# Performance work log

Measured on AMD Instinct MI355X. Metric: run time of the kernel, lower is better.

Reference implementation:

```python
import jax, jax.numpy as jnp
import numpy as np

B, T, V, E, H, NC = 256, 512, 128, 128, 256, 10000


def setup_inputs() -> dict:
    key = jax.random.key(0)
    ks = jax.random.split(key, 10)
    return {
        "dec_input_batch": jax.random.randint(ks[0], (B, T), 0, V),
        "dec_input_lengths": jax.random.randint(ks[1], (B,), 1, T + 1),
        "max_prob_clusters": jax.random.randint(ks[2], (B,), 0, NC),
        "char_embeddings": jax.random.normal(ks[3], (V, E), dtype=jnp.float32) * 0.1,
        "cluster_embeddings": jax.random.normal(ks[4], (NC, H), dtype=jnp.float32) * 0.1,
        "W0": jax.random.normal(ks[5], (E + H + H, 4 * H), dtype=jnp.float32) * 0.05,
        "b0": jnp.zeros((4 * H,), jnp.float32),
        "W1": jax.random.normal(ks[6], (H + H, 4 * H), dtype=jnp.float32) * 0.05,
        "b1": jnp.zeros((4 * H,), jnp.float32),
        "decoderW": jax.random.normal(ks[7], (H, V), dtype=jnp.float32) * (1.0 / (H + V)),
        "decoderB": jnp.zeros((V,), jnp.float32),
    }


def _lstm_step(c, h, x, W, b):
    # TF BasicLSTMCell: gates order i, j, f, o; forget_bias = 1.0
    z = jnp.concatenate([x, h], axis=-1) @ W + b
    i, j, f, o = jnp.split(z, 4, axis=-1)
    c2 = c * jax.nn.sigmoid(f + 1.0) + jax.nn.sigmoid(i) * jnp.tanh(j)
    h2 = jnp.tanh(c2) * jax.nn.sigmoid(o)
    return c2, h2


def reference(dec_input_batch, dec_input_lengths, max_prob_clusters,
              char_embeddings, cluster_embeddings, W0, b0, W1, b1,
              decoderW, decoderB):
    Bb, Tt = dec_input_batch.shape
    Hh = decoderW.shape[0]
    x = char_embeddings[dec_input_batch]                       # [B,T,E]
    clus = cluster_embeddings[max_prob_clusters]               # [B,H]
    clus_bt = jnp.broadcast_to(clus[:, None, :], (Bb, Tt, clus.shape[-1]))
    x = jnp.concatenate([x, clus_bt], axis=-1)                 # [B,T,E+H]
    xs = jnp.transpose(x, (1, 0, 2))                           # [T,B,E+H]
    # dynamic_rnn sequence_length semantics: past length -> zero output, state copied through
    mask = (jnp.arange(Tt)[:, None] < dec_input_lengths[None, :])[..., None]  # [T,B,1]
    zeros = jnp.zeros((Bb, Hh), x.dtype)

    def step(carry, inp):
        c0, h0, c1, h1 = carry
        xt, m = inp
        c0n, h0n = _lstm_step(c0, h0, xt, W0, b0)
        c1n, h1n = _lstm_step(c1, h1, h0n, W1, b1)
        c0 = jnp.where(m, c0n, c0); h0 = jnp.where(m, h0n, h0)
        c1 = jnp.where(m, c1n, c1); h1 = jnp.where(m, h1n, h1)
        out = jnp.where(m, h1n, jnp.zeros_like(h1n))
        return (c0, h0, c1, h1), out

    _, outs = jax.lax.scan(step, (zeros, zeros, zeros, zeros), (xs, mask))
    outs = jnp.transpose(outs, (1, 0, 2))                      # [B,T,H]
    raw_scores = outs @ decoderW + decoderB                    # [B,T,V]
    return raw_scores
```

## Files before the change

### kernel.cpp

```cpp
#include <hip/hip_runtime.h>

#define B_ 256
#define T_ 512
#define V_ 128
#define E_ 128
#define H_ 256
#define FH 1024

#define GROUPS 32
#define RPG 8
#define CWG 16
#define NWG (GROUPS*CWG)

#define HTG (H_*RPG)
#define GST (GROUPS*HTG)

typedef float f4 __attribute__((ext_vector_type(4)));

#define OFF_HT0  0
#define OFF_HT1  (OFF_HT0 + 2*GST)
#define OFF_BAR  (OFF_HT1 + 2*GST)
#define OFF_TP   (OFF_BAR + 4096)
#define OFF_CP   (OFF_TP + V_*FH)
#define OFF_WP0  (OFF_CP + B_*FH)
#define OFF_WP1  (OFF_WP0 + CWG*64*64*4)
#define OFF_DWT  (OFF_WP1 + CWG*128*64*4)
#define OFF_B1   (OFF_DWT + V_*H_)

__device__ __forceinline__ int gcol(int c, int col) {
  int u = col >> 2, g = col & 3;
  return g*256 + c*16 + u;
}

__device__ __forceinline__ float sigm(float x){ return 1.f/(1.f+__expf(-x)); }
__device__ __forceinline__ float tanh_(float x){ return 1.f - 2.f/(1.f+__expf(2.f*x)); }


__global__ void prep_pack(const float* __restrict__ W0, const float* __restrict__ W1,
                          const float* __restrict__ dW, const float* __restrict__ b1,
                          float* __restrict__ ws) {
  float* wp0 = ws + OFF_WP0; float* wp1 = ws + OFF_WP1;
  float* dwT = ws + OFF_DWT; float* b1p = ws + OFF_B1;
  const int N0 = CWG*64*64*4;
  const int N1 = CWG*128*64*4;
  const int N2 = V_*H_;
  const int N3 = FH;
  const int total = N0+N1+N2+N3;
  for (int i = blockIdx.x*blockDim.x + threadIdx.x; i < total; i += gridDim.x*blockDim.x) {
    if (i < N0) {
      int cc = i >> 14; int rem = i & 16383;
      int kb = rem >> 8; int ln = (rem >> 2) & 63; int j = i & 3;
      int k = kb*4 + j;
      wp0[i] = W0[(E_+H_+k)*FH + gcol(cc, ln)];
    } else if (i < N0+N1) {
      int idx = i - N0;
      int cc = idx >> 15; int rem = idx & 32767;
      int kb = rem >> 8; int ln = (rem >> 2) & 63; int j = idx & 3;
      int k2 = kb*4 + j;
      wp1[idx] = W1[k2*FH + gcol(cc, ln)];
    } else if (i < N0+N1+N2) {
      int l = i - N0 - N1;
      int v = l >> 8, k = l & 255;
      dwT[l] = dW[k*V_ + v];
    } else {
      int cc2 = i - N0 - N1 - N2;
      b1p[cc2] = b1[gcol(cc2>>6, cc2&63)];
    }
  }
}

__global__ void prep_tok(const float* __restrict__ cemb, const float* __restrict__ W0,
                         float* __restrict__ ws) {
  __shared__ float ce[E_];
  float* TP = ws + OFF_TP;
  int v = blockIdx.x >> 2, q = blockIdx.x & 3;
  int tid = threadIdx.x;
  if (tid < E_) ce[tid] = cemb[v*E_ + tid];
  __syncthreads();
  int ccol = q*256 + tid;
  int G = gcol(ccol>>6, ccol&63);
  float acc = 0.f;
  for (int e = 0; e < E_; ++e) acc = fmaf(ce[e], W0[e*FH + G], acc);
  TP[v*FH + ccol] = acc;
}

__global__ void prep_clus(const int* __restrict__ clus, const float* __restrict__ clemb,
                          const float* __restrict__ W0, const float* __restrict__ b0,
                          float* __restrict__ ws) {
  __shared__ float ce[H_];
  float* CP = ws + OFF_CP;
  int b = blockIdx.x >> 2, q = blockIdx.x & 3;
  int tid = threadIdx.x;
  int cl = clus[b];
  ce[tid] = clemb[(long long)cl*H_ + tid];
  __syncthreads();
  int ccol = q*256 + tid;
  int G = gcol(ccol>>6, ccol&63);
  float acc = b0[G];
  for (int e = 0; e < H_; ++e) acc = fmaf(ce[e], W0[(E_+e)*FH + G], acc);
  CP[b*FH + ccol] = acc;
}


__device__ __forceinline__ void st_coh(float* p, float v) {
  __hip_atomic_store(p, v, __ATOMIC_RELAXED, __HIP_MEMORY_SCOPE_AGENT);
}

__device__ __forceinline__ void stage_row(const float* g, float* l) {
  const unsigned long long* p = (const unsigned long long*)g;
  unsigned long long d0 = __hip_atomic_load(p+0, __ATOMIC_RELAXED, __HIP_MEMORY_SCOPE_AGENT);
  unsigned long long d1 = __hip_atomic_load(p+1, __ATOMIC_RELAXED, __HIP_MEMORY_SCOPE_AGENT);
  unsigned long long d2 = __hip_atomic_load(p+2, __ATOMIC_RELAXED, __HIP_MEMORY_SCOPE_AGENT);
  unsigned long long d3 = __hip_atomic_load(p+3, __ATOMIC_RELAXED, __HIP_MEMORY_SCOPE_AGENT);
  float2 f0 = __builtin_bit_cast(float2, d0);
  float2 f1 = __builtin_bit_cast(float2, d1);
  float2 f2 = __builtin_bit_cast(float2, d2);
  float2 f3 = __builtin_bit_cast(float2, d3);
  f4 lo = {f0.x, f0.y, f1.x, f1.y};
  f4 hi = {f2.x, f2.y, f3.x, f3.y};
  *(f4*)(l)     = lo;
  *(f4*)(l + 4) = hi;
}

__device__ __forceinline__ void flag_set(unsigned* p, unsigned v) {
  asm volatile("s_waitcnt vmcnt(0)" ::: "memory");
  __hip_atomic_store(p, v, __ATOMIC_RELAXED, __HIP_MEMORY_SCOPE_AGENT);
}

__device__ __forceinline__ void spinAB(const unsigned* fA, const unsigned* fB,
                                       int lane, unsigned tgt) {
  const unsigned* p = ((lane < 32) ? fA : fB) + (lane & 15);
  unsigned v = __hip_atomic_load(p, __ATOMIC_RELAXED, __HIP_MEMORY_SCOPE_AGENT);
  while (!__all((int)(v >= tgt))) {
    __builtin_amdgcn_s_sleep(2);
    v = __hip_atomic_load(p, __ATOMIC_RELAXED, __HIP_MEMORY_SCOPE_AGENT);
  }
}

__device__ __forceinline__ void spin1(const unsigned* f, int lane, unsigned tgt) {
  const unsigned* p = f + (lane & 15);
  unsigned v = __hip_atomic_load(p, __ATOMIC_RELAXED, __HIP_MEMORY_SCOPE_AGENT);
  while (!__all((int)(v >= tgt))) {
    __builtin_amdgcn_s_sleep(2);
    v = __hip_atomic_load(p, __ATOMIC_RELAXED, __HIP_MEMORY_SCOPE_AGENT);
  }
}

__device__ __forceinline__ void lstm_gate(const f4 z, float& cc, float& hh, const bool upd) {
  float ci = sigm(z.x);
  float cj = tanh_(z.y);
  float cf = sigm(z.z + 1.f);
  float co = sigm(z.w);
  float cn = fmaf(cc, cf, ci*cj);
  float hn = tanh_(cn)*co;
  if (upd) { cc = cn; hh = hn; }
}


__global__ __launch_bounds__(256, 2) void lstm_persist(
    const int* __restrict__ toks, const int* __restrict__ lens,
    const float* __restrict__ decB, float* __restrict__ ws, float* __restrict__ out)
{
  const int blk  = blockIdx.x;
  const int grp  = ((blk & 7) << 2) | ((blk >> 3) >> 4);
  const int c    = (blk >> 3) & 15;
  const int tid  = threadIdx.x;
  const int lane = tid & 63;
  const int wv   = tid >> 6;
  const int cof  = c*64;

  float* ht0 = ws + OFF_HT0;
  float* ht1 = ws + OFF_HT1;
  unsigned* fgrp = (unsigned*)(ws + OFF_BAR) + grp*128;
  unsigned* fA = fgrp;
  unsigned* fB = fgrp + 32;
  const float* TP   = ws + OFF_TP;
  const float* CP   = ws + OFF_CP;
  const float* wp0c = ws + OFF_WP0 + c*(64*64*4);
  const float* wp1c = ws + OFF_WP1 + c*(128*64*4);
  const float* dwT  = ws + OFF_DWT;
  const float* b1p  = ws + OFF_B1;

  __shared__ __align__(16) float h0s[256][8];
  __shared__ __align__(16) float h1s[256][8];
  __shared__ float za[4][8][64];
  __shared__ float zb[4][8][64];
  __shared__ float ldsW[8][260];
  __shared__ float pred[4][64];

  for (int i = tid; i < 8*H_; i += 256)
    ldsW[i>>8][i&255] = dwT[(c*8 + (i>>8))*H_ + (i&255)];

  const int sk = (tid + (c << 4)) & 255;

  int Lg = lens[grp*RPG + (lane & 7)];
  Lg = max(Lg, __shfl_xor(Lg, 1));
  Lg = max(Lg, __shfl_xor(Lg, 2));
  Lg = max(Lg, __shfl_xor(Lg, 4));

  const int gu = lane & 15, q = lane >> 4;
  const int rowA = grp*RPG + q, rowB = grp*RPG + q + 4;
  const int lenA = lens[rowA], lenB = lens[rowB];
  const int* tokApt = toks + rowA*T_;
  const int* tokBpt = toks + rowB*T_;
  const f4 cpA = *(const f4*)(CP + rowA*FH + cof + gu*4);
  const f4 cpB = *(const f4*)(CP + rowB*FH + cof + gu*4);
  const f4 b1v = *(const f4*)(b1p + cof + gu*4);
  const int puboff = grp*HTG + (c*16 + gu)*8;
  float c0A = 0.f, h0A = 0.f, c0B = 0.f, h0B = 0.f;
  float c1A = 0.f, h1A = 0.f, c1B = 0.f, h1B = 0.f;

  const int pm = lane >> 3, pv = lane & 7;
  const int plen = lens[grp*RPG + pm];
  const float decb = decB[c*8 + pv];
  float* outp = out + (size_t)(grp*RPG + pm)*T_*V_ + c*8 + pv;

  float a0[8], a1[8];

  __syncthreads();

  if (wv == 0) {
    int tokA = tokApt[0], tokB = tokBpt[0];
    f4 zA = *(const f4*)(TP + tokA*FH + cof + gu*4) + cpA;
    f4 zB = *(const f4*)(TP + tokB*FH + cof + gu*4) + cpB;
    lstm_gate(zA, c0A, h0A, 0 < lenA);
    lstm_gate(zB, c0B, h0B, 0 < lenB);
    float* pb = ht0 + puboff;
    st_coh(pb + q,     h0A);
    st_coh(pb + q + 4, h0B);
    if (lane == 0) flag_set(fA + c, 1u);
  } else if (wv == 1) {
    if (lane == 0) flag_set(fB + c, 1u);
  }

  for (int t = 0; t < Lg; ++t) {
    const int buf = t & 1;

    if (wv == 0) spinAB(fA, fB, lane, (unsigned)(t + 1));
    __syncthreads();
    __atomic_signal_fence(__ATOMIC_SEQ_CST);

    f4 tpA = {0.f,0.f,0.f,0.f}, tpB = {0.f,0.f,0.f,0.f};
    if (wv == 0 && t + 1 < Lg) {
      tpA = *(const f4*)(TP + tokApt[t+1]*FH + cof + gu*4);
      tpB = *(const f4*)(TP + tokBpt[t+1]*FH + cof + gu*4);
    }

    stage_row(ht0 + buf*GST + grp*HTG + sk*8, &h0s[sk][0]);
    stage_row(ht1 + buf*GST + grp*HTG + sk*8, &h1s[sk][0]);
    __syncthreads();

    #pragma unroll
    for (int r = 0; r < 8; ++r) { a0[r] = 0.f; a1[r] = 0.f; }
    #pragma unroll 2
    for (int b = 0; b < 16; ++b) {
      const int kb = wv*16 + b;
      const f4 w0  = *(const f4*)(wp0c + kb*256 + lane*4);
      const f4 wlo = *(const f4*)(wp1c + kb*256 + lane*4);
      const f4 wup = *(const f4*)(wp1c + (64 + kb)*256 + lane*4);
      const float* w0a  = (const float*)&w0;
      const float* wloa = (const float*)&wlo;
      const float* wupa = (const float*)&wup;
      #pragma unroll
      for (int j = 0; j < 4; ++j) {
        const int k = kb*4 + j;
        const f4 h0a = *(const f4*)&h0s[k][0];
        const f4 h0b = *(const f4*)&h0s[k][4];
        const f4 h1a = *(const f4*)&h1s[k][0];
        const f4 h1b = *(const f4*)&h1s[k][4];
        const float w0j = w0a[j], wlj = wloa[j], wuj = wupa[j];
        a0[0]=fmaf(w0j,h0a.x,a0[0]); a0[1]=fmaf(w0j,h0a.y,a0[1]);
        a0[2]=fmaf(w0j,h0a.z,a0[2]); a0[3]=fmaf(w0j,h0a.w,a0[3]);
        a0[4]=fmaf(w0j,h0b.x,a0[4]); a0[5]=fmaf(w0j,h0b.y,a0[5]);
        a0[6]=fmaf(w0j,h0b.z,a0[6]); a0[7]=fmaf(w0j,h0b.w,a0[7]);
        a1[0]=fmaf(wlj,h0a.x,a1[0]); a1[1]=fmaf(wlj,h0a.y,a1[1]);
        a1[2]=fmaf(wlj,h0a.z,a1[2]); a1[3]=fmaf(wlj,h0a.w,a1[3]);
        a1[4]=fmaf(wlj,h0b.x,a1[4]); a1[5]=fmaf(wlj,h0b.y,a1[5]);
        a1[6]=fmaf(wlj,h0b.z,a1[6]); a1[7]=fmaf(wlj,h0b.w,a1[7]);
        a1[0]=fmaf(wuj,h1a.x,a1[0]); a1[1]=fmaf(wuj,h1a.y,a1[1]);
        a1[2]=fmaf(wuj,h1a.z,a1[2]); a1[3]=fmaf(wuj,h1a.w,a1[3]);
        a1[4]=fmaf(wuj,h1b.x,a1[4]); a1[5]=fmaf(wuj,h1b.y,a1[5]);
        a1[6]=fmaf(wuj,h1b.z,a1[6]); a1[7]=fmaf(wuj,h1b.w,a1[7]);
      }
    }

    float pacc = 0.f;
    {
      const int kq = wv*64;
      #pragma unroll 4
      for (int k2 = 0; k2 < 64; k2 += 4) {
        const f4 w4 = *(const f4*)&ldsW[pv][kq + k2];
        pacc = fmaf(h1s[kq+k2  ][pm], w4.x, pacc);
        pacc = fmaf(h1s[kq+k2+1][pm], w4.y, pacc);
        pacc = fmaf(h1s[kq+k2+2][pm], w4.z, pacc);
        pacc = fmaf(h1s[kq+k2+3][pm], w4.w, pacc);
      }
    }

    #pragma unroll
    for (int r = 0; r < 8; ++r) { za[wv][r][lane] = a0[r]; zb[wv][r][lane] = a1[r]; }
    pred[wv][lane] = pacc;
    __syncthreads();

    if (wv == 0) {
      if (t + 1 < Lg) {
        f4 sA = *(const f4*)&za[0][q][gu*4];
        sA += *(const f4*)&za[1][q][gu*4];
        sA += *(const f4*)&za[2][q][gu*4];
        sA += *(const f4*)&za[3][q][gu*4];
        f4 sB = *(const f4*)&za[0][q+4][gu*4];
        sB += *(const f4*)&za[1][q+4][gu*4];
        sB += *(const f4*)&za[2][q+4][gu*4];
        sB += *(const f4*)&za[3][q+4][gu*4];
        f4 zA = sA + tpA + cpA;
        f4 zB = sB + tpB + cpB;
        lstm_gate(zA, c0A, h0A, (t+1) < lenA);
        lstm_gate(zB, c0B, h0B, (t+1) < lenB);
        float* pb = ht0 + (buf^1)*GST + puboff;
        st_coh(pb + q,     h0A);
        st_coh(pb + q + 4, h0B);
        if (lane == 0) flag_set(fA + c, (unsigned)(t + 2));
      }
    } else if (wv == 1) {
      f4 sA = *(const f4*)&zb[0][q][gu*4];
      sA += *(const f4*)&zb[1][q][gu*4];
      sA += *(const f4*)&zb[2][q][gu*4];
      sA += *(const f4*)&zb[3][q][gu*4];
      f4 sB = *(const f4*)&zb[0][q+4][gu*4];
      sB += *(const f4*)&zb[1][q+4][gu*4];
      sB += *(const f4*)&zb[2][q+4][gu*4];
      sB += *(const f4*)&zb[3][q+4][gu*4];
      f4 zA = sA + b1v;
      f4 zB = sB + b1v;
      lstm_gate(zA, c1A, h1A, t < lenA);
      lstm_gate(zB, c1B, h1B, t < lenB);
      float* pb = ht1 + (buf^1)*GST + puboff;
      st_coh(pb + q,     h1A);
      st_coh(pb + q + 4, h1B);
      if (lane == 0) flag_set(fB + c, (unsigned)(t + 2));
    } else if (wv == 2) {
      if (t > 0) {
        float tot = pred[0][lane] + pred[1][lane] + pred[2][lane] + pred[3][lane] + decb;
        if (t - 1 < plen) outp[(size_t)(t-1)*V_] = tot;
      }
    }
  }

  if (wv == 0) spin1(fB, lane, (unsigned)(Lg + 1));
  __syncthreads();
  __atomic_signal_fence(__ATOMIC_SEQ_CST);
  stage_row(ht1 + (Lg & 1)*GST + grp*HTG + sk*8, &h1s[sk][0]);
  __syncthreads();
  {
    float pacc = 0.f;
    const int kq = wv*64;
    #pragma unroll 4
    for (int k2 = 0; k2 < 64; k2 += 4) {
      const f4 w4 = *(const f4*)&ldsW[pv][kq + k2];
      pacc = fmaf(h1s[kq+k2  ][pm], w4.x, pacc);
      pacc = fmaf(h1s[kq+k2+1][pm], w4.y, pacc);
      pacc = fmaf(h1s[kq+k2+2][pm], w4.z, pacc);
      pacc = fmaf(h1s[kq+k2+3][pm], w4.w, pacc);
    }
    pred[wv][lane] = pacc;
  }
  __syncthreads();
  if (wv == 2) {
    float tot = pred[0][lane] + pred[1][lane] + pred[2][lane] + pred[3][lane] + decb;
    if (Lg - 1 < plen) outp[(size_t)(Lg-1)*V_] = tot;
  }
}


extern "C" void kernel_launch(void* const* d_in, const int* in_sizes, int n_in,
                              void* d_out, int out_size, void* d_ws, size_t ws_size,
                              hipStream_t stream) {
  const int*   toks  = (const int*)d_in[0];
  const int*   lens  = (const int*)d_in[1];
  const int*   clus  = (const int*)d_in[2];
  const float* cemb  = (const float*)d_in[3];
  const float* clemb = (const float*)d_in[4];
  const float* W0    = (const float*)d_in[5];
  const float* b0    = (const float*)d_in[6];
  const float* W1    = (const float*)d_in[7];
  const float* b1    = (const float*)d_in[8];
  const float* dW    = (const float*)d_in[9];
  const float* decB  = (const float*)d_in[10];
  float* out = (float*)d_out;
  float* ws  = (float*)d_ws;

  hipMemsetAsync(out, 0, (size_t)B_*T_*V_*sizeof(float), stream);
  hipMemsetAsync(ws, 0, (size_t)(OFF_BAR + 4096)*sizeof(float), stream);

  prep_pack<<<1024, 256, 0, stream>>>(W0, W1, dW, b1, ws);
  prep_tok <<<V_*4, 256, 0, stream>>>(cemb, W0, ws);
  prep_clus<<<B_*4, 256, 0, stream>>>(clus, clemb, W0, b0, ws);
  lstm_persist<<<NWG, 256, 0, stream>>>(toks, lens, decB, ws, out);
}
```

Before: 5.507 ms.

## Split batch into 64 groups of 4 rows across 1024 persistent workgroups

Halves the rows each workgroup handles, from 8 to 4, and doubles the number of groups and workgroups from 512 to 1024. Occupancy rises to 4 blocks per CU, and the LDS staging, accumulators and output projection shrink to match. The aim is to shorten the serial per-timestep critical path by giving each block half the FMA work. Because each group now takes the max sequence length over only 4 rows, short groups also stop their recurrence earlier. In exchange, every block streams the per-column weight slice each step, so twice as many blocks read weights. The persistent spin-wait scheme also now depends on all 1024 blocks being co-resident.

Result: slower. 6.797 ms (+23.4%).

```diff
diff --git a/kernel.cpp b/kernel.cpp
--- a/kernel.cpp
+++ b/kernel.cpp
@@ -7,8 +7,8 @@
 #define H_ 256
 #define FH 1024
 
-#define GROUPS 32
-#define RPG 8
+#define GROUPS 64
+#define RPG 4
 #define CWG 16
 #define NWG (GROUPS*CWG)
 
@@ -20,7 +20,8 @@
 #define OFF_HT0  0
 #define OFF_HT1  (OFF_HT0 + 2*GST)
 #define OFF_BAR  (OFF_HT1 + 2*GST)
-#define OFF_TP   (OFF_BAR + 4096)
+#define BARSZ    (GROUPS*128)
+#define OFF_TP   (OFF_BAR + BARSZ)
 #define OFF_CP   (OFF_TP + V_*FH)
 #define OFF_WP0  (OFF_CP + B_*FH)
 #define OFF_WP1  (OFF_WP0 + CWG*64*64*4)
@@ -106,20 +107,14 @@
   __hip_atomic_store(p, v, __ATOMIC_RELAXED, __HIP_MEMORY_SCOPE_AGENT);
 }
 
-__device__ __forceinline__ void stage_row(const float* g, float* l) {
+__device__ __forceinline__ void stage16(const float* g, float* l) {
   const unsigned long long* p = (const unsigned long long*)g;
   unsigned long long d0 = __hip_atomic_load(p+0, __ATOMIC_RELAXED, __HIP_MEMORY_SCOPE_AGENT);
   unsigned long long d1 = __hip_atomic_load(p+1, __ATOMIC_RELAXED, __HIP_MEMORY_SCOPE_AGENT);
-  unsigned long long d2 = __hip_atomic_load(p+2, __ATOMIC_RELAXED, __HIP_MEMORY_SCOPE_AGENT);
-  unsigned long long d3 = __hip_atomic_load(p+3, __ATOMIC_RELAXED, __HIP_MEMORY_SCOPE_AGENT);
   float2 f0 = __builtin_bit_cast(float2, d0);
   float2 f1 = __builtin_bit_cast(float2, d1);
-  float2 f2 = __builtin_bit_cast(float2, d2);
-  float2 f3 = __builtin_bit_cast(float2, d3);
-  f4 lo = {f0.x, f0.y, f1.x, f1.y};
-  f4 hi = {f2.x, f2.y, f3.x, f3.y};
-  *(f4*)(l)     = lo;
-  *(f4*)(l + 4) = hi;
+  f4 v = {f0.x, f0.y, f1.x, f1.y};
+  *(f4*)(l) = v;
 }
 
 __device__ __forceinline__ void flag_set(unsigned* p, unsigned v) {
@@ -157,13 +152,13 @@
 }
 
 
-__global__ __launch_bounds__(256, 2) void lstm_persist(
+__global__ __launch_bounds__(256, 4) void lstm_persist(
     const int* __restrict__ toks, const int* __restrict__ lens,
     const float* __restrict__ decB, float* __restrict__ ws, float* __restrict__ out)
 {
   const int blk  = blockIdx.x;
-  const int grp  = ((blk & 7) << 2) | ((blk >> 3) >> 4);
-  const int c    = (blk >> 3) & 15;
+  const int grp  = (blk & 7)*8 + ((blk >> 3) & 7);
+  const int c    = blk >> 6;
   const int tid  = threadIdx.x;
   const int lane = tid & 63;
   const int wv   = tid >> 6;
@@ -181,53 +176,46 @@
   const float* dwT  = ws + OFF_DWT;
   const float* b1p  = ws + OFF_B1;
 
-  __shared__ __align__(16) float h0s[256][8];
-  __shared__ __align__(16) float h1s[256][8];
-  __shared__ float za[4][8][64];
-  __shared__ float zb[4][8][64];
+  __shared__ __align__(16) float h0s[256][4];
+  __shared__ __align__(16) float h1s[256][4];
+  __shared__ float za[4][4][64];
+  __shared__ float zb[4][4][64];
   __shared__ float ldsW[8][260];
-  __shared__ float pred[4][64];
+  __shared__ float pred[8][32];
 
   for (int i = tid; i < 8*H_; i += 256)
     ldsW[i>>8][i&255] = dwT[(c*8 + (i>>8))*H_ + (i&255)];
 
   const int sk = (tid + (c << 4)) & 255;
 
-  int Lg = lens[grp*RPG + (lane & 7)];
+  int Lg = lens[grp*RPG + (lane & 3)];
   Lg = max(Lg, __shfl_xor(Lg, 1));
   Lg = max(Lg, __shfl_xor(Lg, 2));
-  Lg = max(Lg, __shfl_xor(Lg, 4));
 
   const int gu = lane & 15, q = lane >> 4;
-  const int rowA = grp*RPG + q, rowB = grp*RPG + q + 4;
-  const int lenA = lens[rowA], lenB = lens[rowB];
+  const int rowA = grp*RPG + q;
+  const int lenA = lens[rowA];
   const int* tokApt = toks + rowA*T_;
-  const int* tokBpt = toks + rowB*T_;
   const f4 cpA = *(const f4*)(CP + rowA*FH + cof + gu*4);
-  const f4 cpB = *(const f4*)(CP + rowB*FH + cof + gu*4);
   const f4 b1v = *(const f4*)(b1p + cof + gu*4);
-  const int puboff = grp*HTG + (c*16 + gu)*8;
-  float c0A = 0.f, h0A = 0.f, c0B = 0.f, h0B = 0.f;
-  float c1A = 0.f, h1A = 0.f, c1B = 0.f, h1B = 0.f;
-
-  const int pm = lane >> 3, pv = lane & 7;
+  const int puboff = grp*HTG + (c*16 + gu)*4 + q;
+  float c0A = 0.f, h0A = 0.f;
+  float c1A = 0.f, h1A = 0.f;
+
+  const int half = lane >> 5, pm = (lane >> 3) & 3, pv = lane & 7;
   const int plen = lens[grp*RPG + pm];
   const float decb = decB[c*8 + pv];
   float* outp = out + (size_t)(grp*RPG + pm)*T_*V_ + c*8 + pv;
 
-  float a0[8], a1[8];
+  float a0[4], a1[4];
 
   __syncthreads();
 
   if (wv == 0) {
-    int tokA = tokApt[0], tokB = tokBpt[0];
+    int tokA = tokApt[0];
     f4 zA = *(const f4*)(TP + tokA*FH + cof + gu*4) + cpA;
-    f4 zB = *(const f4*)(TP + tokB*FH + cof + gu*4) + cpB;
     lstm_gate(zA, c0A, h0A, 0 < lenA);
-    lstm_gate(zB, c0B, h0B, 0 < lenB);
-    float* pb = ht0 + puboff;
-    st_coh(pb + q,     h0A);
-    st_coh(pb + q + 4, h0B);
+    st_coh(ht0 + puboff, h0A);
     if (lane == 0) flag_set(fA + c, 1u);
   } else if (wv == 1) {
     if (lane == 0) flag_set(fB + c, 1u);
@@ -240,18 +228,16 @@
     __syncthreads();
     __atomic_signal_fence(__ATOMIC_SEQ_CST);
 
-    f4 tpA = {0.f,0.f,0.f,0.f}, tpB = {0.f,0.f,0.f,0.f};
-    if (wv == 0 && t + 1 < Lg) {
+    f4 tpA = {0.f,0.f,0.f,0.f};
+    if (wv == 0 && t + 1 < Lg)
       tpA = *(const f4*)(TP + tokApt[t+1]*FH + cof + gu*4);
-      tpB = *(const f4*)(TP + tokBpt[t+1]*FH + cof + gu*4);
-    }
-
-    stage_row(ht0 + buf*GST + grp*HTG + sk*8, &h0s[sk][0]);
-    stage_row(ht1 + buf*GST + grp*HTG + sk*8, &h1s[sk][0]);
+
+    stage16(ht0 + buf*GST + grp*HTG + sk*4, &h0s[sk][0]);
+    stage16(ht1 + buf*GST + grp*HTG + sk*4, &h1s[sk][0]);
     __syncthreads();
 
     #pragma unroll
-    for (int r = 0; r < 8; ++r) { a0[r] = 0.f; a1[r] = 0.f; }
+    for (int r = 0; r < 4; ++r) { a0[r] = 0.f; a1[r] = 0.f; }
     #pragma unroll 2
     for (int b = 0; b < 16; ++b) {
       const int kb = wv*16 + b;
@@ -264,31 +250,23 @@
       #pragma unroll
       for (int j = 0; j < 4; ++j) {
         const int k = kb*4 + j;
-        const f4 h0a = *(const f4*)&h0s[k][0];
-        const f4 h0b = *(const f4*)&h0s[k][4];
-        const f4 h1a = *(const f4*)&h1s[k][0];
-        const f4 h1b = *(const f4*)&h1s[k][4];
+        const f4 h0v = *(const f4*)&h0s[k][0];
+        const f4 h1v = *(const f4*)&h1s[k][0];
         const float w0j = w0a[j], wlj = wloa[j], wuj = wupa[j];
-        a0[0]=fmaf(w0j,h0a.x,a0[0]); a0[1]=fmaf(w0j,h0a.y,a0[1]);
-        a0[2]=fmaf(w0j,h0a.z,a0[2]); a0[3]=fmaf(w0j,h0a.w,a0[3]);
-        a0[4]=fmaf(w0j,h0b.x,a0[4]); a0[5]=fmaf(w0j,h0b.y,a0[5]);
-        a0[6]=fmaf(w0j,h0b.z,a0[6]); a0[7]=fmaf(w0j,h0b.w,a0[7]);
-        a1[0]=fmaf(wlj,h0a.x,a1[0]); a1[1]=fmaf(wlj,h0a.y,a1[1]);
-        a1[2]=fmaf(wlj,h0a.z,a1[2]); a1[3]=fmaf(wlj,h0a.w,a1[3]);
-        a1[4]=fmaf(wlj,h0b.x,a1[4]); a1[5]=fmaf(wlj,h0b.y,a1[5]);
-        a1[6]=fmaf(wlj,h0b.z,a1[6]); a1[7]=fmaf(wlj,h0b.w,a1[7]);
-        a1[0]=fmaf(wuj,h1a.x,a1[0]); a1[1]=fmaf(wuj,h1a.y,a1[1]);
-        a1[2]=fmaf(wuj,h1a.z,a1[2]); a1[3]=fmaf(wuj,h1a.w,a1[3]);
-        a1[4]=fmaf(wuj,h1b.x,a1[4]); a1[5]=fmaf(wuj,h1b.y,a1[5]);
-        a1[6]=fmaf(wuj,h1b.z,a1[6]); a1[7]=fmaf(wuj,h1b.w,a1[7]);
+        a0[0]=fmaf(w0j,h0v.x,a0[0]); a0[1]=fmaf(w0j,h0v.y,a0[1]);
+        a0[2]=fmaf(w0j,h0v.z,a0[2]); a0[3]=fmaf(w0j,h0v.w,a0[3]);
+        a1[0]=fmaf(wlj,h0v.x,a1[0]); a1[1]=fmaf(wlj,h0v.y,a1[1]);
+        a1[2]=fmaf(wlj,h0v.z,a1[2]); a1[3]=fmaf(wlj,h0v.w,a1[3]);
+        a1[0]=fmaf(wuj,h1v.x,a1[0]); a1[1]=fmaf(wuj,h1v.y,a1[1]);
+        a1[2]=fmaf(wuj,h1v.z,a1[2]); a1[3]=fmaf(wuj,h1v.w,a1[3]);
       }
     }
 
     float pacc = 0.f;
     {
-      const int kq = wv*64;
-      #pragma unroll 4
-      for (int k2 = 0; k2 < 64; k2 += 4) {
+      const int kq = wv*64 + half*32;
+      #pragma unroll 8
+      for (int k2 = 0; k2 < 32; k2 += 4) {
         const f4 w4 = *(const f4*)&ldsW[pv][kq + k2];
         pacc = fmaf(h1s[kq+k2  ][pm], w4.x, pacc);
         pacc = fmaf(h1s[kq+k2+1][pm], w4.y, pacc);
@@ -298,8 +276,8 @@
     }
 
     #pragma unroll
-    for (int r = 0; r < 8; ++r) { za[wv][r][lane] = a0[r]; zb[wv][r][lane] = a1[r]; }
-    pred[wv][lane] = pacc;
+    for (int r = 0; r < 4; ++r) { za[wv][r][lane] = a0[r]; zb[wv][r][lane] = a1[r]; }
+    pred[wv*2 + half][lane & 31] = pacc;
     __syncthreads();
 
     if (wv == 0) {
@@ -308,17 +286,9 @@
         sA += *(const f4*)&za[1][q][gu*4];
         sA += *(const f4*)&za[2][q][gu*4];
         sA += *(const f4*)&za[3][q][gu*4];
-        f4 sB = *(const f4*)&za[0][q+4][gu*4];
-        sB += *(const f4*)&za[1][q+4][gu*4];
-        sB += *(const f4*)&za[2][q+4][gu*4];
-        sB += *(const f4*)&za[3][q+4][gu*4];
         f4 zA = sA + tpA + cpA;
-        f4 zB = sB + tpB + cpB;
         lstm_gate(zA, c0A, h0A, (t+1) < lenA);
-        lstm_gate(zB, c0B, h0B, (t+1) < lenB);
-        float* pb = ht0 + (buf^1)*GST + puboff;
-        st_coh(pb + q,     h0A);
-        st_coh(pb + q + 4, h0B);
+        st_coh(ht0 + (buf^1)*GST + puboff, h0A);
         if (lane == 0) flag_set(fA + c, (unsigned)(t + 2));
       }
     } else if (wv == 1) {
@@ -326,21 +296,15 @@
       sA += *(const f4*)&zb[1][q][gu*4];
       sA += *(const f4*)&zb[2][q][gu*4];
       sA += *(const f4*)&zb[3][q][gu*4];
-      f4 sB = *(const f4*)&zb[0][q+4][gu*4];
-      sB += *(const f4*)&zb[1][q+4][gu*4];
-      sB += *(const f4*)&zb[2][q+4][gu*4];
-      sB += *(const f4*)&zb[3][q+4][gu*4];
       f4 zA = sA + b1v;
-      f4 zB = sB + b1v;
       lstm_gate(zA, c1A, h1A, t < lenA);
-      lstm_gate(zB, c1B, h1B, t < lenB);
-      float* pb = ht1 + (buf^1)*GST + puboff;
-      st_coh(pb + q,     h1A);
-      st_coh(pb + q + 4, h1B);
+      st_coh(ht1 + (buf^1)*GST + puboff, h1A);
       if (lane == 0) flag_set(fB + c, (unsigned)(t + 2));
     } else if (wv == 2) {
-      if (t > 0) {
-        float tot = pred[0][lane] + pred[1][lane] + pred[2][lane] + pred[3][lane] + decb;
+      if (t > 0 && lane < 32) {
+        float tot = decb;
+        #pragma unroll
+        for (int p = 0; p < 8; ++p) tot += pred[p][lane];
         if (t - 1 < plen) outp[(size_t)(t-1)*V_] = tot;
       }
     }
@@ -349,24 +313,26 @@
   if (wv == 0) spin1(fB, lane, (unsigned)(Lg + 1));
   __syncthreads();
   __atomic_signal_fence(__ATOMIC_SEQ_CST);
-  stage_row(ht1 + (Lg & 1)*GST + grp*HTG + sk*8, &h1s[sk][0]);
+  stage16(ht1 + (Lg & 1)*GST + grp*HTG + sk*4, &h1s[sk][0]);
   __syncthreads();
   {
     float pacc = 0.f;
-    const int kq = wv*64;
-    #pragma unroll 4
-    for (int k2 = 0; k2 < 64; k2 += 4) {
+    const int kq = wv*64 + half*32;
+    #pragma unroll 8
+    for (int k2 = 0; k2 < 32; k2 += 4) {
       const f4 w4 = *(const f4*)&ldsW[pv][kq + k2];
       pacc = fmaf(h1s[kq+k2  ][pm], w4.x, pacc);
       pacc = fmaf(h1s[kq+k2+1][pm], w4.y, pacc);
       pacc = fmaf(h1s[kq+k2+2][pm], w4.z, pacc);
       pacc = fmaf(h1s[kq+k2+3][pm], w4.w, pacc);
     }
-    pred[wv][lane] = pacc;
-  }
-  __syncthreads();
-  if (wv == 2) {
-    float tot = pred[0][lane] + pred[1][lane] + pred[2][lane] + pred[3][lane] + decb;
+    pred[wv*2 + half][lane & 31] = pacc;
+  }
+  __syncthreads();
+  if (wv == 2 && lane < 32) {
+    float tot = decb;
+    #pragma unroll
+    for (int p = 0; p < 8; ++p) tot += pred[p][lane];
     if (Lg - 1 < plen) outp[(size_t)(Lg-1)*V_] = tot;
   }
 }
@@ -390,7 +356,7 @@
   float* ws  = (float*)d_ws;
 
   hipMemsetAsync(out, 0, (size_t)B_*T_*V_*sizeof(float), stream);
-  hipMemsetAsync(ws, 0, (size_t)(OFF_BAR + 4096)*sizeof(float), stream);
+  hipMemsetAsync(ws, 0, (size_t)(OFF_BAR + BARSZ)*sizeof(float), stream);
 
   prep_pack<<<1024, 256, 0, stream>>>(W0, W1, dW, b1, ws);
   prep_tok <<<V_*4, 256, 0, stream>>>(cemb, W0, ws);
```

## Pad flags to separate lines, drop staging barrier, pack h publishes into 64-bit stores

Applied to the files above, without the earlier changes.

Each per-column readiness flag for layer 0 and layer 1 now sits on its own cache line instead of sharing one. Hidden-state publishes pack the two batch rows into a single 64-bit atomic store. Each wave stages from global memory exactly the slice of h it later reads, which removes the __syncthreads between staging and the matvec. The next-token table loads are issued before the spin-wait, and the spin sleep is lengthened. The aim is less false sharing and polling traffic, fewer barriers and fewer stores on the serial per-step critical path, at the cost of a larger flag region and coarser polling granularity.

Measured after the change: 5.421 ms. About the same (-1.6%).

```diff
diff --git a/kernel.cpp b/kernel.cpp
--- a/kernel.cpp
+++ b/kernel.cpp
@@ -12,7 +12,7 @@
 #define CWG 16
 #define NWG (GROUPS*CWG)
 
-#define HTG (H_*RPG)
+#define HTG 2048
 #define GST (GROUPS*HTG)
 
 typedef float f4 __attribute__((ext_vector_type(4)));
@@ -20,7 +20,8 @@
 #define OFF_HT0  0
 #define OFF_HT1  (OFF_HT0 + 2*GST)
 #define OFF_BAR  (OFF_HT1 + 2*GST)
-#define OFF_TP   (OFF_BAR + 4096)
+#define BARSZ    (GROUPS*1024)
+#define OFF_TP   (OFF_BAR + BARSZ)
 #define OFF_CP   (OFF_TP + V_*FH)
 #define OFF_WP0  (OFF_CP + B_*FH)
 #define OFF_WP1  (OFF_WP0 + CWG*64*64*4)
@@ -102,24 +103,15 @@
 }
 
 
-__device__ __forceinline__ void st_coh(float* p, float v) {
-  __hip_atomic_store(p, v, __ATOMIC_RELAXED, __HIP_MEMORY_SCOPE_AGENT);
-}
-
-__device__ __forceinline__ void stage_row(const float* g, float* l) {
-  const unsigned long long* p = (const unsigned long long*)g;
-  unsigned long long d0 = __hip_atomic_load(p+0, __ATOMIC_RELAXED, __HIP_MEMORY_SCOPE_AGENT);
-  unsigned long long d1 = __hip_atomic_load(p+1, __ATOMIC_RELAXED, __HIP_MEMORY_SCOPE_AGENT);
-  unsigned long long d2 = __hip_atomic_load(p+2, __ATOMIC_RELAXED, __HIP_MEMORY_SCOPE_AGENT);
-  unsigned long long d3 = __hip_atomic_load(p+3, __ATOMIC_RELAXED, __HIP_MEMORY_SCOPE_AGENT);
-  float2 f0 = __builtin_bit_cast(float2, d0);
-  float2 f1 = __builtin_bit_cast(float2, d1);
-  float2 f2 = __builtin_bit_cast(float2, d2);
-  float2 f3 = __builtin_bit_cast(float2, d3);
-  f4 lo = {f0.x, f0.y, f1.x, f1.y};
-  f4 hi = {f2.x, f2.y, f3.x, f3.y};
-  *(f4*)(l)     = lo;
-  *(f4*)(l + 4) = hi;
+__device__ __forceinline__ void st64(float* p, float a, float b) {
+  float2 t; t.x = a; t.y = b;
+  __hip_atomic_store((unsigned long long*)p, __builtin_bit_cast(unsigned long long, t),
+                     __ATOMIC_RELAXED, __HIP_MEMORY_SCOPE_AGENT);
+}
+
+__device__ __forceinline__ unsigned long long ld64(const void* p) {
+  return __hip_atomic_load((const unsigned long long*)p, __ATOMIC_RELAXED,
+                           __HIP_MEMORY_SCOPE_AGENT);
 }
 
 __device__ __forceinline__ void flag_set(unsigned* p, unsigned v) {
@@ -127,21 +119,20 @@
   __hip_atomic_store(p, v, __ATOMIC_RELAXED, __HIP_MEMORY_SCOPE_AGENT);
 }
 
-__device__ __forceinline__ void spinAB(const unsigned* fA, const unsigned* fB,
-                                       int lane, unsigned tgt) {
-  const unsigned* p = ((lane < 32) ? fA : fB) + (lane & 15);
+__device__ __forceinline__ void spinAB(const unsigned* fgrp, int lane, unsigned tgt) {
+  const unsigned* p = fgrp + (lane & 15)*32 + ((lane >> 5) << 4);
   unsigned v = __hip_atomic_load(p, __ATOMIC_RELAXED, __HIP_MEMORY_SCOPE_AGENT);
   while (!__all((int)(v >= tgt))) {
-    __builtin_amdgcn_s_sleep(2);
+    __builtin_amdgcn_s_sleep(4);
     v = __hip_atomic_load(p, __ATOMIC_RELAXED, __HIP_MEMORY_SCOPE_AGENT);
   }
 }
 
-__device__ __forceinline__ void spin1(const unsigned* f, int lane, unsigned tgt) {
-  const unsigned* p = f + (lane & 15);
+__device__ __forceinline__ void spinB(const unsigned* fgrp, int lane, unsigned tgt) {
+  const unsigned* p = fgrp + (lane & 15)*32 + 16;
   unsigned v = __hip_atomic_load(p, __ATOMIC_RELAXED, __HIP_MEMORY_SCOPE_AGENT);
   while (!__all((int)(v >= tgt))) {
-    __builtin_amdgcn_s_sleep(2);
+    __builtin_amdgcn_s_sleep(4);
     v = __hip_atomic_load(p, __ATOMIC_RELAXED, __HIP_MEMORY_SCOPE_AGENT);
   }
 }
@@ -162,7 +153,7 @@
     const float* __restrict__ decB, float* __restrict__ ws, float* __restrict__ out)
 {
   const int blk  = blockIdx.x;
-  const int grp  = ((blk & 7) << 2) | ((blk >> 3) >> 4);
+  const int grp  = ((blk & 7) << 2) | (blk >> 7);
   const int c    = (blk >> 3) & 15;
   const int tid  = threadIdx.x;
   const int lane = tid & 63;
@@ -171,9 +162,7 @@
 
   float* ht0 = ws + OFF_HT0;
   float* ht1 = ws + OFF_HT1;
-  unsigned* fgrp = (unsigned*)(ws + OFF_BAR) + grp*128;
-  unsigned* fA = fgrp;
-  unsigned* fB = fgrp + 32;
+  unsigned* fgrp = (unsigned*)(ws + OFF_BAR) + grp*1024;
   const float* TP   = ws + OFF_TP;
   const float* CP   = ws + OFF_CP;
   const float* wp0c = ws + OFF_WP0 + c*(64*64*4);
@@ -181,17 +170,15 @@
   const float* dwT  = ws + OFF_DWT;
   const float* b1p  = ws + OFF_B1;
 
-  __shared__ __align__(16) float h0s[256][8];
-  __shared__ __align__(16) float h1s[256][8];
-  __shared__ float za[4][8][64];
-  __shared__ float zb[4][8][64];
+  __shared__ __align__(16) float h0s[2048];
+  __shared__ __align__(16) float h1s[2048];
+  __shared__ __align__(16) float za[4][8][64];
+  __shared__ __align__(16) float zb[4][8][64];
   __shared__ float ldsW[8][260];
   __shared__ float pred[4][64];
 
   for (int i = tid; i < 8*H_; i += 256)
     ldsW[i>>8][i&255] = dwT[(c*8 + (i>>8))*H_ + (i&255)];
-
-  const int sk = (tid + (c << 4)) & 255;
 
   int Lg = lens[grp*RPG + (lane & 7)];
   Lg = max(Lg, __shfl_xor(Lg, 1));
@@ -206,81 +193,77 @@
   const f4 cpA = *(const f4*)(CP + rowA*FH + cof + gu*4);
   const f4 cpB = *(const f4*)(CP + rowB*FH + cof + gu*4);
   const f4 b1v = *(const f4*)(b1p + cof + gu*4);
-  const int puboff = grp*HTG + (c*16 + gu)*8;
+  const int puboff = grp*HTG + (c*16 + gu)*8 + q*2;
   float c0A = 0.f, h0A = 0.f, c0B = 0.f, h0B = 0.f;
   float c1A = 0.f, h1A = 0.f, c1B = 0.f, h1B = 0.f;
 
   const int pm = lane >> 3, pv = lane & 7;
+  const int prm = (pm < 4) ? pm*2 : (pm-4)*2 + 1;
   const int plen = lens[grp*RPG + pm];
   const float decb = decB[c*8 + pv];
   float* outp = out + (size_t)(grp*RPG + pm)*T_*V_ + c*8 + pv;
 
-  float a0[8], a1[8];
-
   __syncthreads();
 
   if (wv == 0) {
-    int tokA = tokApt[0], tokB = tokBpt[0];
-    f4 zA = *(const f4*)(TP + tokA*FH + cof + gu*4) + cpA;
-    f4 zB = *(const f4*)(TP + tokB*FH + cof + gu*4) + cpB;
-    lstm_gate(zA, c0A, h0A, 0 < lenA);
-    lstm_gate(zB, c0B, h0B, 0 < lenB);
-    float* pb = ht0 + puboff;
-    st_coh(pb + q,     h0A);
-    st_coh(pb + q + 4, h0B);
-    if (lane == 0) flag_set(fA + c, 1u);
+    f4 zAv = *(const f4*)(TP + tokApt[0]*FH + cof + gu*4) + cpA;
+    f4 zBv = *(const f4*)(TP + tokBpt[0]*FH + cof + gu*4) + cpB;
+    lstm_gate(zAv, c0A, h0A, 0 < lenA);
+    lstm_gate(zBv, c0B, h0B, 0 < lenB);
+    st64(ht0 + puboff, h0A, h0B);
+    if (lane == 0) flag_set(fgrp + c*32, 1u);
   } else if (wv == 1) {
-    if (lane == 0) flag_set(fB + c, 1u);
+    if (lane == 0) flag_set(fgrp + c*32 + 16, 1u);
   }
 
   for (int t = 0; t < Lg; ++t) {
     const int buf = t & 1;
 
-    if (wv == 0) spinAB(fA, fB, lane, (unsigned)(t + 1));
-    __syncthreads();
-    __atomic_signal_fence(__ATOMIC_SEQ_CST);
-
-    f4 tpA = {0.f,0.f,0.f,0.f}, tpB = {0.f,0.f,0.f,0.f};
+    f4 tpA = {0,0,0,0}, tpB = {0,0,0,0};
     if (wv == 0 && t + 1 < Lg) {
       tpA = *(const f4*)(TP + tokApt[t+1]*FH + cof + gu*4);
       tpB = *(const f4*)(TP + tokBpt[t+1]*FH + cof + gu*4);
     }
 
-    stage_row(ht0 + buf*GST + grp*HTG + sk*8, &h0s[sk][0]);
-    stage_row(ht1 + buf*GST + grp*HTG + sk*8, &h1s[sk][0]);
+    if (wv == 0) spinAB(fgrp, lane, (unsigned)(t + 1));
     __syncthreads();
-
-    #pragma unroll
-    for (int r = 0; r < 8; ++r) { a0[r] = 0.f; a1[r] = 0.f; }
+    __atomic_signal_fence(__ATOMIC_SEQ_CST);
+
+    {
+      const float* s0 = ht0 + buf*GST + grp*HTG + wv*512 + lane*8;
+      const float* s1 = ht1 + buf*GST + grp*HTG + wv*512 + lane*8;
+      unsigned long long a0 = ld64(s0),   a1 = ld64(s0+2);
+      unsigned long long a2 = ld64(s0+4), a3 = ld64(s0+6);
+      unsigned long long b0 = ld64(s1),   b1 = ld64(s1+2);
+      unsigned long long b2 = ld64(s1+4), b3 = ld64(s1+6);
+      float* d0 = h0s + wv*512 + lane*8;
+      float* d1 = h1s + wv*512 + lane*8;
+      *(unsigned long long*)(d0)   = a0; *(unsigned long long*)(d0+2) = a1;
+      *(unsigned long long*)(d0+4) = a2; *(unsigned long long*)(d0+6) = a3;
+      *(unsigned long long*)(d1)   = b0; *(unsigned long long*)(d1+2) = b1;
+      *(unsigned long long*)(d1+4) = b2; *(unsigned long long*)(d1+6) = b3;
+    }
+
+    f4 A0l = {0,0,0,0}, A0h = {0,0,0,0}, A1l = {0,0,0,0}, A1h = {0,0,0,0};
     #pragma unroll 2
     for (int b = 0; b < 16; ++b) {
       const int kb = wv*16 + b;
-      const f4 w0  = *(const f4*)(wp0c + kb*256 + lane*4);
-      const f4 wlo = *(const f4*)(wp1c + kb*256 + lane*4);
-      const f4 wup = *(const f4*)(wp1c + (64 + kb)*256 + lane*4);
-      const float* w0a  = (const float*)&w0;
-      const float* wloa = (const float*)&wlo;
-      const float* wupa = (const float*)&wup;
+      const f4 w0 = *(const f4*)(wp0c + kb*256 + lane*4);
+      const f4 wl = *(const f4*)(wp1c + kb*256 + lane*4);
+      const f4 wu = *(const f4*)(wp1c + (64 + kb)*256 + lane*4);
       #pragma unroll
       for (int j = 0; j < 4; ++j) {
         const int k = kb*4 + j;
-        const f4 h0a = *(const f4*)&h0s[k][0];
-        const f4 h0b = *(const f4*)&h0s[k][4];
-        const f4 h1a = *(const f4*)&h1s[k][0];
-        const f4 h1b = *(const f4*)&h1s[k][4];
-        const float w0j = w0a[j], wlj = wloa[j], wuj = wupa[j];
-        a0[0]=fmaf(w0j,h0a.x,a0[0]); a0[1]=fmaf(w0j,h0a.y,a0[1]);
-        a0[2]=fmaf(w0j,h0a.z,a0[2]); a0[3]=fmaf(w0j,h0a.w,a0[3]);
-        a0[4]=fmaf(w0j,h0b.x,a0[4]); a0[5]=fmaf(w0j,h0b.y,a0[5]);
-        a0[6]=fmaf(w0j,h0b.z,a0[6]); a0[7]=fmaf(w0j,h0b.w,a0[7]);
-        a1[0]=fmaf(wlj,h0a.x,a1[0]); a1[1]=fmaf(wlj,h0a.y,a1[1]);
-        a1[2]=fmaf(wlj,h0a.z,a1[2]); a1[3]=fmaf(wlj,h0a.w,a1[3]);
-        a1[4]=fmaf(wlj,h0b.x,a1[4]); a1[5]=fmaf(wlj,h0b.y,a1[5]);
-        a1[6]=fmaf(wlj,h0b.z,a1[6]); a1[7]=fmaf(wlj,h0b.w,a1[7]);
-        a1[0]=fmaf(wuj,h1a.x,a1[0]); a1[1]=fmaf(wuj,h1a.y,a1[1]);
-        a1[2]=fmaf(wuj,h1a.z,a1[2]); a1[3]=fmaf(wuj,h1a.w,a1[3]);
-        a1[4]=fmaf(wuj,h1b.x,a1[4]); a1[5]=fmaf(wuj,h1b.y,a1[5]);
-        a1[6]=fmaf(wuj,h1b.z,a1[6]); a1[7]=fmaf(wuj,h1b.w,a1[7]);
+        const float* hb0 = h0s + k*8;
+        const float* hb1 = h1s + k*8;
+        const f4 h0lo = *(const f4*)(hb0);
+        const f4 h0hi = *(const f4*)(hb0 + 4);
+        const f4 h1lo = *(const f4*)(hb1);
+        const f4 h1hi = *(const f4*)(hb1 + 4);
+        const float w0j = w0[j], wlj = wl[j], wuj = wu[j];
+        A0l += w0j * h0lo;  A0h += w0j * h0hi;
+        A1l += wlj * h0lo + wuj * h1lo;
+        A1h += wlj * h0hi + wuj * h1hi;
       }
     }
 
@@ -290,54 +273,55 @@
       #pragma unroll 4
       for (int k2 = 0; k2 < 64; k2 += 4) {
         const f4 w4 = *(const f4*)&ldsW[pv][kq + k2];
-        pacc = fmaf(h1s[kq+k2  ][pm], w4.x, pacc);
-        pacc = fmaf(h1s[kq+k2+1][pm], w4.y, pacc);
-        pacc = fmaf(h1s[kq+k2+2][pm], w4.z, pacc);
-        pacc = fmaf(h1s[kq+k2+3][pm], w4.w, pacc);
+        pacc = fmaf(h1s[(kq+k2  )*8 + prm], w4.x, pacc);
+        pacc = fmaf(h1s[(kq+k2+1)*8 + prm], w4.y, pacc);
+        pacc = fmaf(h1s[(kq+k2+2)*8 + prm], w4.z, pacc);
+        pacc = fmaf(h1s[(kq+k2+3)*8 + prm], w4.w, pacc);
       }
     }
 
     #pragma unroll
-    for (int r = 0; r < 8; ++r) { za[wv][r][lane] = a0[r]; zb[wv][r][lane] = a1[r]; }
+    for (int r = 0; r < 4; ++r) {
+      za[wv][r][lane]     = A0l[r];
+      za[wv][4 + r][lane] = A0h[r];
+      zb[wv][r][lane]     = A1l[r];
+      zb[wv][4 + r][lane] = A1h[r];
+    }
     pred[wv][lane] = pacc;
     __syncthreads();
 
     if (wv == 0) {
       if (t + 1 < Lg) {
-        f4 sA = *(const f4*)&za[0][q][gu*4];
-        sA += *(const f4*)&za[1][q][gu*4];
-        sA += *(const f4*)&za[2][q][gu*4];
-        sA += *(const f4*)&za[3][q][gu*4];
-        f4 sB = *(const f4*)&za[0][q+4][gu*4];
-        sB += *(const f4*)&za[1][q+4][gu*4];
-        sB += *(const f4*)&za[2][q+4][gu*4];
-        sB += *(const f4*)&za[3][q+4][gu*4];
-        f4 zA = sA + tpA + cpA;
-        f4 zB = sB + tpB + cpB;
+        f4 zA = *(const f4*)&za[0][q*2][gu*4];
+        zA += *(const f4*)&za[1][q*2][gu*4];
+        zA += *(const f4*)&za[2][q*2][gu*4];
+        zA += *(const f4*)&za[3][q*2][gu*4];
+        f4 zB = *(const f4*)&za[0][q*2+1][gu*4];
+        zB += *(const f4*)&za[1][q*2+1][gu*4];
+        zB += *(const f4*)&za[2][q*2+1][gu*4];
+        zB += *(const f4*)&za[3][q*2+1][gu*4];
+        zA += tpA + cpA;
+        zB += tpB + cpB;
         lstm_gate(zA, c0A, h0A, (t+1) < lenA);
         lstm_gate(zB, c0B, h0B, (t+1) < lenB);
-        float* pb = ht0 + (buf^1)*GST + puboff;
-        st_coh(pb + q,     h0A);
-        st_coh(pb + q + 4, h0B);
-        if (lane == 0) flag_set(fA + c, (unsigned)(t + 2));
+        st64(ht0 + (buf^1)*GST + puboff, h0A, h0B);
+        if (lane == 0) flag_set(fgrp + c*32, (unsigned)(t + 2));
       }
     } else if (wv == 1) {
-      f4 sA = *(const f4*)&zb[0][q][gu*4];
-      sA += *(const f4*)&zb[1][q][gu*4];
-      sA += *(const f4*)&zb[2][q][gu*4];
-      sA += *(const f4*)&zb[3][q][gu*4];
-      f4 sB = *(const f4*)&zb[0][q+4][gu*4];
-      sB += *(const f4*)&zb[1][q+4][gu*4];
-      sB += *(const f4*)&zb[2][q+4][gu*4];
-      sB += *(const f4*)&zb[3][q+4][gu*4];
-      f4 zA = sA + b1v;
-      f4 zB = sB + b1v;
+      f4 zA = *(const f4*)&zb[0][q*2][gu*4];
+      zA += *(const f4*)&zb[1][q*2][gu*4];
+      zA += *(const f4*)&zb[2][q*2][gu*4];
+      zA += *(const f4*)&zb[3][q*2][gu*4];
+      f4 zB = *(const f4*)&zb[0][q*2+1][gu*4];
+      zB += *(const f4*)&zb[1][q*2+1][gu*4];
+      zB += *(const f4*)&zb[2][q*2+1][gu*4];
+      zB += *(const f4*)&zb[3][q*2+1][gu*4];
+      zA += b1v;
+      zB += b1v;
       lstm_gate(zA, c1A, h1A, t < lenA);
       lstm_gate(zB, c1B, h1B, t < lenB);
-      float* pb = ht1 + (buf^1)*GST + puboff;
-      st_coh(pb + q,     h1A);
-      st_coh(pb + q + 4, h1B);
-      if (lane == 0) flag_set(fB + c, (unsigned)(t + 2));
+      st64(ht1 + (buf^1)*GST + puboff, h1A, h1B);
+      if (lane == 0) flag_set(fgrp + c*32 + 16, (unsigned)(t + 2));
     } else if (wv == 2) {
       if (t > 0) {
         float tot = pred[0][lane] + pred[1][lane] + pred[2][lane] + pred[3][lane] + decb;
@@ -346,21 +330,27 @@
     }
   }
 
-  if (wv == 0) spin1(fB, lane, (unsigned)(Lg + 1));
+  if (wv == 0) spinB(fgrp, lane, (unsigned)(Lg + 1));
   __syncthreads();
   __atomic_signal_fence(__ATOMIC_SEQ_CST);
-  stage_row(ht1 + (Lg & 1)*GST + grp*HTG + sk*8, &h1s[sk][0]);
-  __syncthreads();
+  {
+    const float* s1 = ht1 + (size_t)(Lg & 1)*GST + grp*HTG + wv*512 + lane*8;
+    unsigned long long b0 = ld64(s1),   b1 = ld64(s1+2);
+    unsigned long long b2 = ld64(s1+4), b3 = ld64(s1+6);
+    float* d1 = h1s + wv*512 + lane*8;
+    *(unsigned long long*)(d1)   = b0; *(unsigned long long*)(d1+2) = b1;
+    *(unsigned long long*)(d1+4) = b2; *(unsigned long long*)(d1+6) = b3;
+  }
   {
     float pacc = 0.f;
     const int kq = wv*64;
     #pragma unroll 4
     for (int k2 = 0; k2 < 64; k2 += 4) {
       const f4 w4 = *(const f4*)&ldsW[pv][kq + k2];
-      pacc = fmaf(h1s[kq+k2  ][pm], w4.x, pacc);
-      pacc = fmaf(h1s[kq+k2+1][pm], w4.y, pacc);
-      pacc = fmaf(h1s[kq+k2+2][pm], w4.z, pacc);
-      pacc = fmaf(h1s[kq+k2+3][pm], w4.w, pacc);
+      pacc = fmaf(h1s[(kq+k2  )*8 + prm], w4.x, pacc);
+      pacc = fmaf(h1s[(kq+k2+1)*8 + prm], w4.y, pacc);
+      pacc = fmaf(h1s[(kq+k2+2)*8 + prm], w4.z, pacc);
+      pacc = fmaf(h1s[(kq+k2+3)*8 + prm], w4.w, pacc);
     }
     pred[wv][lane] = pacc;
   }
@@ -390,7 +380,7 @@
   float* ws  = (float*)d_ws;
 
   hipMemsetAsync(out, 0, (size_t)B_*T_*V_*sizeof(float), stream);
-  hipMemsetAsync(ws, 0, (size_t)(OFF_BAR + 4096)*sizeof(float), stream);
+  hipMemsetAsync(ws, 0, (size_t)(OFF_BAR + BARSZ)*sizeof(float), stream);
 
   prep_pack<<<1024, 256, 0, stream>>>(W0, W1, dW, b1, ws);
   prep_tok <<<V_*4, 256, 0, stream>>>(cemb, W0, ws);
```
